# Kernel tuning notes

Hardware: AMD Instinct MI355X
Metric: run time of the kernel (lower is better)

## Reference

```python
import jax, jax.numpy as jnp
import numpy as np

B, N, D = 4, 2048, 512
H = 8            # num_heads (even)
HE = H // 2      # effective heads = 4
DH = D // H      # head_dim = 64
LAMBDA_INIT = 0.8
EPS = 1e-5


def setup_inputs() -> dict:
    key = jax.random.key(0)
    ks = jax.random.split(key, 10)
    return {
        "q": jax.random.normal(ks[0], (B, N, D), jnp.float32),
        "k": jax.random.normal(ks[1], (B, N, D), jnp.float32),
        "v": jax.random.normal(ks[2], (B, N, D), jnp.float32),
        "lambda_q1": 0.1 * jax.random.normal(ks[3], (DH,), jnp.float32),
        "lambda_k1": 0.1 * jax.random.normal(ks[4], (DH,), jnp.float32),
        "lambda_q2": 0.1 * jax.random.normal(ks[5], (DH,), jnp.float32),
        "lambda_k2": 0.1 * jax.random.normal(ks[6], (DH,), jnp.float32),
        "norm_w": jnp.ones((2 * DH,), jnp.float32),
        "out_w": 0.02 * jax.random.normal(ks[7], (D, D), jnp.float32),  # torch Linear weight [out,in]
        "out_b": jnp.zeros((D,), jnp.float32),
    }


def reference(q, k, v, lambda_q1, lambda_k1, lambda_q2, lambda_k2, norm_w, out_w, out_b):
    b, nq, d = q.shape
    nk = k.shape[1]
    # split heads: q,k -> [B, 2*HE, N, DH]; v -> [B, HE, Nk, 2*DH]
    qh = q.reshape(b, nq, 2 * HE, DH).transpose(0, 2, 1, 3) * (DH ** -0.5)
    kh = k.reshape(b, nk, 2 * HE, DH).transpose(0, 2, 1, 3)
    vh = v.reshape(b, nk, HE, 2 * DH).transpose(0, 2, 1, 3)
    scores = jnp.einsum('bhqd,bhkd->bhqk', qh, kh)          # [B, 2HE, Nq, Nk]
    probs = jax.nn.softmax(scores, axis=-1)
    probs = probs.reshape(b, HE, 2, nq, nk)
    lam = (jnp.exp(jnp.sum(lambda_q1 * lambda_k1))
           - jnp.exp(jnp.sum(lambda_q2 * lambda_k2)) + LAMBDA_INIT)
    diff = probs[:, :, 0] - lam * probs[:, :, 1]            # [B, HE, Nq, Nk]
    out = jnp.einsum('bhqk,bhkd->bhqd', diff, vh)           # [B, HE, Nq, 2*DH]
    # per-head RMSNorm over last dim (2*DH), elementwise affine
    out = out * jax.lax.rsqrt(jnp.mean(out * out, axis=-1, keepdims=True) + EPS)
    out = out * norm_w * (1.0 - LAMBDA_INIT)
    out = out.transpose(0, 2, 1, 3).reshape(b, nq, d)
    return out @ out_w.T + out_b
```

## Files before the change

kernel.cpp:

```cpp
#include <hip/hip_runtime.h>
#include <math.h>

#define BB 4
#define NN 2048
#define DD 512
#define LAMBDA_INIT 0.8f
#define EPSV 1e-5f

typedef __attribute__((ext_vector_type(8))) short bf16x8;
typedef __attribute__((ext_vector_type(4))) float f32x4;
typedef __attribute__((ext_vector_type(16))) float f32x16;
typedef unsigned short u16;
typedef __attribute__((ext_vector_type(4))) u16 u16x4;
typedef __attribute__((ext_vector_type(8))) u16 u16x8;
typedef __attribute__((ext_vector_type(4))) unsigned u32x4;

__device__ __forceinline__ u16 f2bf(float f) {
  unsigned u = __builtin_bit_cast(unsigned, f);
  u = (u + 0x7FFFu + ((u >> 16) & 1u)) >> 16;
  return (u16)u;
}

__device__ __forceinline__ void gload16(const void* g, void* l) {
  __builtin_amdgcn_global_load_lds((const __attribute__((address_space(1))) unsigned*)g,
                                   (__attribute__((address_space(3))) unsigned*)l, 16, 0, 0);
}

__device__ __forceinline__ f32x16 fz16() {
  f32x16 z;
  #pragma unroll
  for (int i = 0; i < 16; ++i) z[i] = 0.f;
  return z;
}

__device__ __forceinline__ void plswap(unsigned &a, unsigned &b) {
  asm("v_permlane32_swap_b32 %0, %1" : "+v"(a), "+v"(b));
}
__device__ __forceinline__ float xhalf_add(float x) {
  unsigned a = __builtin_bit_cast(unsigned, x), b;
  asm("v_mov_b32 %0, %1" : "=v"(b) : "v"(a));
  asm("v_permlane32_swap_b32 %0, %1" : "+v"(a), "+v"(b));
  return __builtin_bit_cast(float, a) + __builtin_bit_cast(float, b);
}

__global__ __launch_bounds__(256) void prep_kernel(
    const float* __restrict__ q, const float* __restrict__ k, const float* __restrict__ w,
    u16* __restrict__ Qb, u16* __restrict__ Kb, u16* __restrict__ Wb)
{
  const int t = threadIdx.x;
  const int bid = blockIdx.x;
  if (bid >= BB * NN) {
    const size_t idx = (size_t)(bid - BB * NN) * 256 + t;
    float4 f = *(const float4*)&w[idx * 4];
    u16x4 o = { f2bf(f.x), f2bf(f.y), f2bf(f.z), f2bf(f.w) };
    *(u16x4*)&Wb[idx * 4] = o;
    return;
  }
  const size_t row = bid;
  const int n = bid & (NN - 1);
  const int b = bid >> 11;
  if (t < 128) {
    const float s = 0.125f * 1.4426950408889634f;
    float4 f = *(const float4*)&q[row * DD + t * 4];
    u16x4 o = { f2bf(f.x * s), f2bf(f.y * s), f2bf(f.z * s), f2bf(f.w * s) };
    *(u16x4*)&Qb[row * DD + t * 4] = o;
  } else {
    const int f0 = (t - 128) * 4;
    float4 f = *(const float4*)&k[row * DD + f0];
    const int he = f0 >> 7, fi = f0 & 127;
    const int gi = fi >> 3, lo = fi & 7;
    const int gi2 = (gi & 8) | ((gi & 7) ^ (n & 7));
    u16x4 o = { f2bf(f.x), f2bf(f.y), f2bf(f.z), f2bf(f.w) };
    *(u16x4*)&Kb[((size_t)(b * 4 + he) * NN + n) * 128 + gi2 * 8 + lo] = o;
  }
}

__global__ __launch_bounds__(256) void v_prep_kernel(const float* __restrict__ v, u16* __restrict__ Vbt) {
  __shared__ u16 Ls[64][72];
  const int t = threadIdx.x;
  const int n0 = blockIdx.x * 64;
  const int d0 = blockIdx.y * 64;
  const int z  = blockIdx.z;
  #pragma unroll
  for (int p = 0; p < 4; ++p) {
    int n = p * 16 + (t >> 4), f4 = t & 15;
    float4 rv = *(const float4*)&v[((size_t)((z >> 2) * NN + n0 + n)) * DD + (z & 3) * 128 + d0 + f4 * 4];
    Ls[n][f4*4+0] = f2bf(rv.x); Ls[n][f4*4+1] = f2bf(rv.y);
    Ls[n][f4*4+2] = f2bf(rv.z); Ls[n][f4*4+3] = f2bf(rv.w);
  }
  __syncthreads();
  #pragma unroll
  for (int rep = 0; rep < 2; ++rep) {
    const int sid   = rep * 256 + t;
    const int tt    = sid >> 8;
    const int rem   = sid & 255;
    const int i_rel = rem >> 6;
    const int ls    = rem & 63;
    const int i_    = (d0 >> 4) + i_rel;
    const int j     = i_ * 8 + (ls >> 3);
    const int s0    = (ls & 7) ^ (j & 7);
    const int dl    = 2 * (i_rel * 8 + (ls >> 3)) + (s0 >> 2);
    const int nl0   = tt * 32 + (s0 & 3) * 8;
    u16x8 o;
    #pragma unroll
    for (int jj = 0; jj < 8; ++jj) o[jj] = Ls[nl0 + jj][dl];
    const int tile = blockIdx.x * 2 + tt;
    *(u16x8*)&Vbt[((size_t)z * 64 + tile) * 4096 + i_ * 512 + ls * 8] = o;
  }
}

#define ISSUE_K4(dst, kv0, hf) do { \
  _Pragma("unroll") for (int i_ = 0; i_ < 4; ++i_) { int ii_ = (hf)*4 + i_; \
    gload16(kgb + (((size_t)(kv0) + ii_ * 4 + (l >> 4)) << 7) + ((l & 15) << 3), (dst) + ii_ * 512); } \
  __builtin_amdgcn_sched_barrier(0); } while (0)

#define ISSUE_V4(dst, kv0, hf) do { \
  _Pragma("unroll") for (int i_ = 0; i_ < 4; ++i_) { int ii_ = (hf)*4 + i_; \
    gload16(vgb + ((size_t)((kv0) >> 5)) * 4096 + ii_ * 512 + l * 8, (dst) + ii_ * 512); } \
  __builtin_amdgcn_sched_barrier(0); } while (0)

#define WAIT_VM0 do { asm volatile("s_waitcnt vmcnt(0)" ::: "memory"); \
  __builtin_amdgcn_sched_barrier(0); } while (0)

__global__ __launch_bounds__(512, 2) void attn7_kernel(
    const u16* __restrict__ Qb, const u16* __restrict__ Kb, const u16* __restrict__ Vbt,
    const float* __restrict__ lq1, const float* __restrict__ lk1,
    const float* __restrict__ lq2, const float* __restrict__ lk2,
    const float* __restrict__ norm_w, u16* __restrict__ Xb)
{
  __shared__ __align__(16) u16 smem[32768];
  __shared__ float stats[2][2][2][32];

  u16* KB = smem;
  u16* VB = smem + 16384;

  const int tid = threadIdx.x;
  const int w   = tid >> 6;
  const int l   = tid & 63;
  const int hi  = l >> 5;
  const int q   = l & 31;
  const int h   = w & 1;
  const int kvh = (w >> 1) & 1;
  const int qh  = w >> 2;

  const int bid0 = blockIdx.x;
  const int bid = (bid0 & 7) * 64 + (bid0 >> 3);
  const int qt = bid & 31;
  const int he = (bid >> 5) & 3;
  const int b  = bid >> 7;
  const int q0 = qt * 64;
  const int bhe = b * 4 + he;
  const int qrow = q0 + qh * 32 + q;

  float lp1 = lq1[l] * lk1[l], lp2 = lq2[l] * lk2[l];
  #pragma unroll
  for (int off = 32; off; off >>= 1) { lp1 += __shfl_xor(lp1, off); lp2 += __shfl_xor(lp2, off); }
  const float lam = __expf(lp1) - __expf(lp2) + LAMBDA_INIT;
  asm volatile("" :: "v"(lam));

  bf16x8 qf[4];
  {
    const u16* qp = Qb + ((size_t)(b * NN) + qrow) * DD + he * 128 + h * 64 + hi * 8;
    #pragma unroll
    for (int dk = 0; dk < 4; ++dk)
      qf[dk] = *(const bf16x8*)(qp + dk * 16);
  }
  WAIT_VM0;
  #pragma unroll
  for (int dk = 0; dk < 4; ++dk)
    asm volatile("" :: "v"(qf[dk]));

  const u16* kgb = Kb + (size_t)bhe * NN * 128;
  const u16* vgb = Vbt + (size_t)bhe * 64 * 4096;
  const int kvb = kvh * 1024;

  if (h == 0) ISSUE_K4(&KB[kvh * 8192], kvb, qh);
  else        ISSUE_V4(&VB[kvh * 8192], kvb, qh);

  f32x16 O[4];
  #pragma unroll
  for (int dt = 0; dt < 4; ++dt) O[dt] = fz16();
  float sl = 0.f;

  const int jq  = (q >> 1) & 7;
  const int dq1 = (q & 1) << 2;

  #pragma unroll 2
  for (int tt = 0; tt < 32; ++tt) {
    WAIT_VM0;
    __builtin_amdgcn_s_barrier();
    __builtin_amdgcn_sched_barrier(0);

    {
      const int kvn = kvb + ((tt + 1) & 31) * 32;
      const int db = (tt + 1) & 1;
      if (h == 0) ISSUE_K4(&KB[(kvh * 2 + db) * 4096], kvn, qh);
      else        ISSUE_V4(&VB[(kvh * 2 + db) * 4096], kvn, qh);
    }

    const u16* Kcur = &KB[(kvh * 2 + (tt & 1)) * 4096];
    const u16* Vcur = &VB[(kvh * 2 + (tt & 1)) * 4096];

    f32x16 S;
    __builtin_amdgcn_s_setprio(1);
    {
      f32x16 acc = fz16();
      #pragma unroll
      for (int dk = 0; dk < 4; ++dk) {
        const int gd = h * 8 + dk * 2 + hi;
        const int g2 = (gd & 8) | ((gd & 7) ^ (q & 7));
        bf16x8 kf = *(const bf16x8*)&Kcur[q * 128 + g2 * 8];
        acc = __builtin_amdgcn_mfma_f32_32x32x16_bf16(kf, qf[dk], acc, 0, 0, 0);
      }
      S = acc;
    }
    __builtin_amdgcn_s_setprio(0);

    #pragma unroll
    for (int r = 0; r < 16; ++r)
      S[r] = __builtin_amdgcn_exp2f(S[r]);
    {
      float y0 = (S[0]  + S[1])  + (S[2]  + S[3]);
      float y1 = (S[4]  + S[5])  + (S[6]  + S[7]);
      float y2 = (S[8]  + S[9])  + (S[10] + S[11]);
      float y3 = (S[12] + S[13]) + (S[14] + S[15]);
      sl += (y0 + y1) + (y2 + y3);
    }
    bf16x8 pb[2];
    {
      unsigned PK[8];
      #pragma unroll
      for (int p2 = 0; p2 < 8; ++p2)
        asm("v_cvt_pk_bf16_f32 %0, %1, %2" : "=v"(PK[p2]) : "v"(S[2*p2]), "v"(S[2*p2+1]));
      #pragma unroll
      for (int kb = 0; kb < 2; ++kb) {
        unsigned w0 = PK[4*kb + 0], w2v = PK[4*kb + 2];
        unsigned w1 = PK[4*kb + 1], w3v = PK[4*kb + 3];
        plswap(w0, w2v);
        plswap(w1, w3v);
        union { u32x4 u; bf16x8 v; } cv;
        cv.u = (u32x4){ w0, w1, w2v, w3v };
        pb[kb] = cv.v;
      }
    }

    __builtin_amdgcn_s_setprio(1);
    #pragma unroll
    for (int kk = 0; kk < 2; ++kk)
      #pragma unroll
      for (int dt = 0; dt < 4; ++dt) {
        const int j = dt * 16 + (q >> 1);
        const int s8 = (dq1 + kk * 2 + hi) ^ jq;
        bf16x8 vf = *(const bf16x8*)&Vcur[j * 64 + s8 * 8];
        O[dt] = __builtin_amdgcn_mfma_f32_32x32x16_bf16(vf, pb[kk], O[dt], 0, 0, 0);
      }
    __builtin_amdgcn_s_setprio(0);
  }

  WAIT_VM0;
  __syncthreads();

  sl = xhalf_add(sl);
  if (hi == 0) stats[qh][h][kvh][q] = sl;
  __syncthreads();
  const float L = stats[qh][h][0][q] + stats[qh][h][1][q];

  float* xch = (float*)smem;
  if (kvh == 1) {
    #pragma unroll
    for (int dt = 0; dt < 4; ++dt)
      #pragma unroll
      for (int r = 0; r < 16; ++r)
        xch[(qh * 2 + h) * 4096 + (dt * 16 + r) * 64 + l] = O[dt][r];
  }
  __syncthreads();
  if (kvh == 0) {
    #pragma unroll
    for (int dt = 0; dt < 4; ++dt)
      #pragma unroll
      for (int r = 0; r < 16; ++r)
        O[dt][r] += xch[(qh * 2 + h) * 4096 + (dt * 16 + r) * 64 + l];
  }
  __syncthreads();
  if (kvh == 0 && h == 1) {
    const float s2 = lam / L;
    #pragma unroll
    for (int dt = 0; dt < 4; ++dt)
      #pragma unroll
      for (int r = 0; r < 16; ++r)
        xch[qh * 4096 + (dt * 16 + r) * 64 + l] = O[dt][r] * s2;
  }
  __syncthreads();
  if (kvh == 0 && h == 0) {
    const float i1 = 1.f / L;
    float ss = 0.f;
    #pragma unroll
    for (int dt = 0; dt < 4; ++dt)
      #pragma unroll
      for (int r = 0; r < 16; ++r) {
        float o = O[dt][r] * i1 - xch[qh * 4096 + (dt * 16 + r) * 64 + l];
        O[dt][r] = o;
        ss += o * o;
      }
    ss = xhalf_add(ss);
    const float rstd = rsqrtf(ss * (1.f / 128.f) + EPSV);
    const size_t xo = ((size_t)(b * NN) + qrow) * DD + he * 128;
    #pragma unroll
    for (int dt = 0; dt < 4; ++dt)
      #pragma unroll
      for (int rq = 0; rq < 4; ++rq) {
        const int d0 = dt * 32 + rq * 8 + hi * 4;
        const float4 nw = *(const float4*)&norm_w[d0];
        u16x4 ov;
        ov[0] = f2bf(O[dt][rq*4 + 0] * rstd * nw.x * 0.2f);
        ov[1] = f2bf(O[dt][rq*4 + 1] * rstd * nw.y * 0.2f);
        ov[2] = f2bf(O[dt][rq*4 + 2] * rstd * nw.z * 0.2f);
        ov[3] = f2bf(O[dt][rq*4 + 3] * rstd * nw.w * 0.2f);
        *(u16x4*)&Xb[xo + d0] = ov;
      }
  }
}

#define PLOAD(k0) do { \
    _Pragma("unroll") for (int p_ = 0; p_ < 2; ++p_) { \
      int idx_ = p_*256 + t; int r_ = idx_ >> 3, gi_ = idx_ & 7; \
      ra[p_] = *(const u16x8*)&Xb[(size_t)(row0 + r_) * DD + (k0) + gi_*8]; \
      rb[p_] = *(const u16x8*)&Wb[(size_t)(col0 + r_) * DD + (k0) + gi_*8]; } \
  } while (0)
#define PWRITE(bi) do { \
    _Pragma("unroll") for (int p_ = 0; p_ < 2; ++p_) { \
      int idx_ = p_*256 + t; int r_ = idx_ >> 3, gi_ = idx_ & 7; \
      *(u16x8*)&As[bi][r_*64 + ((gi_ ^ (r_ & 7)) << 3)] = ra[p_]; \
      *(u16x8*)&Bs[bi][r_*64 + ((gi_ ^ (r_ & 7)) << 3)] = rb[p_]; } \
  } while (0)

__global__ __launch_bounds__(256, 2) void proj_mfma_kernel(
    const u16* __restrict__ Xb, const u16* __restrict__ Wb,
    const float* __restrict__ bias, float* __restrict__ out)
{
  __shared__ __align__(16) u16 As[2][64*64];
  __shared__ __align__(16) u16 Bs[2][64*64];
  const int t = threadIdx.x;
  const int w = t >> 6, l = t & 63, g = l >> 4, c = l & 15;
  const int wm = w >> 1, wn = w & 1;
  const int row0 = blockIdx.x * 64, col0 = blockIdx.y * 64;

  u16x8 ra[2], rb[2];
  f32x4 acc[2][2];
  #pragma unroll
  for (int i = 0; i < 2; ++i)
    #pragma unroll
    for (int j = 0; j < 2; ++j) acc[i][j] = (f32x4){0,0,0,0};
  float bj[2];
  #pragma unroll
  for (int j = 0; j < 2; ++j) bj[j] = bias[col0 + wn*32 + j*16 + c];

  PLOAD(0);
  PWRITE(0);
  __syncthreads();
  for (int s = 0; s < 8; ++s) {
    const int bi = s & 1;
    if (s < 7) PLOAD((s + 1) * 64);
    #pragma unroll
    for (int kc = 0; kc < 2; ++kc) {
      bf16x8 af[2], bfv[2];
      #pragma unroll
      for (int i = 0; i < 2; ++i) {
        int rowa = wm*32 + i*16 + c;
        af[i]  = *(const bf16x8*)&As[bi][rowa*64 + (((kc*4 + g) ^ (c & 7)) << 3)];
        int rowb = wn*32 + i*16 + c;
        bfv[i] = *(const bf16x8*)&Bs[bi][rowb*64 + (((kc*4 + g) ^ (c & 7)) << 3)];
      }
      #pragma unroll
      for (int i = 0; i < 2; ++i)
        #pragma unroll
        for (int j = 0; j < 2; ++j)
          acc[i][j] = __builtin_amdgcn_mfma_f32_16x16x32_bf16(af[i], bfv[j], acc[i][j], 0, 0, 0);
    }
    if (s < 7) PWRITE((s + 1) & 1);
    __syncthreads();
  }
  #pragma unroll
  for (int i = 0; i < 2; ++i)
    #pragma unroll
    for (int j = 0; j < 2; ++j)
      #pragma unroll
      for (int rr = 0; rr < 4; ++rr)
        out[(size_t)(row0 + wm*32 + i*16 + g*4 + rr) * DD + col0 + wn*32 + j*16 + c] = acc[i][j][rr] + bj[j];
}

extern "C" void kernel_launch(void* const* d_in, const int* in_sizes, int n_in,
                              void* d_out, int out_size, void* d_ws, size_t ws_size,
                              hipStream_t stream) {
    const float* q      = (const float*)d_in[0];
    const float* k      = (const float*)d_in[1];
    const float* v      = (const float*)d_in[2];
    const float* lq1    = (const float*)d_in[3];
    const float* lk1    = (const float*)d_in[4];
    const float* lq2    = (const float*)d_in[5];
    const float* lk2    = (const float*)d_in[6];
    const float* norm_w = (const float*)d_in[7];
    const float* out_w  = (const float*)d_in[8];
    const float* out_b  = (const float*)d_in[9];
    float* out = (float*)d_out;

    u16* Qb  = (u16*)d_ws;
    u16* Kb  = (u16*)((char*)d_ws + (8u  << 20));
    u16* Vbt = (u16*)((char*)d_ws + (16u << 20));
    u16* Wb  = (u16*)((char*)d_ws + (24u << 20));
    u16* Xb  = (u16*)((char*)d_ws + (25u << 20));

    prep_kernel<<<BB * NN + 256, 256, 0, stream>>>(q, k, out_w, Qb, Kb, Wb);
    v_prep_kernel<<<dim3(32, 2, 16), 256, 0, stream>>>(v, Vbt);
    attn7_kernel<<<512, 512, 0, stream>>>(Qb, Kb, Vbt, lq1, lk1, lq2, lk2, norm_w, Xb);
    proj_mfma_kernel<<<dim3(128, 8), 256, 0, stream>>>(Xb, Wb, out_b, out);
}
```

Baseline: 106.7 us.

## Process two query groups per wave to reuse K/V fragments

The attention kernel drops from 8 to 4 waves per block, and each wave now handles both 32-row query groups. Each K and V fragment read from LDS feeds two MFMAs, which halves LDS read traffic per MFMA. The price is doubled accumulator registers, fewer waves available to hide latency, and more complex cross-wave exchange indexing in the epilogue. The loop unroll pragma is removed, likely to limit register pressure.

```diff
diff --git a/kernel.cpp b/kernel.cpp
--- a/kernel.cpp
+++ b/kernel.cpp
@@ -109,20 +109,20 @@
   }
 }
 
-#define ISSUE_K4(dst, kv0, hf) do { \
-  _Pragma("unroll") for (int i_ = 0; i_ < 4; ++i_) { int ii_ = (hf)*4 + i_; \
-    gload16(kgb + (((size_t)(kv0) + ii_ * 4 + (l >> 4)) << 7) + ((l & 15) << 3), (dst) + ii_ * 512); } \
+#define ISSUE_K8(dst, kv0) do { \
+  _Pragma("unroll") for (int i_ = 0; i_ < 8; ++i_) \
+    gload16(kgb + (((size_t)(kv0) + i_ * 4 + (l >> 4)) << 7) + ((l & 15) << 3), (dst) + i_ * 512); \
   __builtin_amdgcn_sched_barrier(0); } while (0)
 
-#define ISSUE_V4(dst, kv0, hf) do { \
-  _Pragma("unroll") for (int i_ = 0; i_ < 4; ++i_) { int ii_ = (hf)*4 + i_; \
-    gload16(vgb + ((size_t)((kv0) >> 5)) * 4096 + ii_ * 512 + l * 8, (dst) + ii_ * 512); } \
+#define ISSUE_V8(dst, kv0) do { \
+  _Pragma("unroll") for (int i_ = 0; i_ < 8; ++i_) \
+    gload16(vgb + ((size_t)((kv0) >> 5)) * 4096 + i_ * 512 + l * 8, (dst) + i_ * 512); \
   __builtin_amdgcn_sched_barrier(0); } while (0)
 
 #define WAIT_VM0 do { asm volatile("s_waitcnt vmcnt(0)" ::: "memory"); \
   __builtin_amdgcn_sched_barrier(0); } while (0)
 
-__global__ __launch_bounds__(512, 2) void attn7_kernel(
+__global__ __launch_bounds__(256, 2) void attn8_kernel(
     const u16* __restrict__ Qb, const u16* __restrict__ Kb, const u16* __restrict__ Vbt,
     const float* __restrict__ lq1, const float* __restrict__ lk1,
     const float* __restrict__ lq2, const float* __restrict__ lk2,
@@ -139,9 +139,8 @@
   const int l   = tid & 63;
   const int hi  = l >> 5;
   const int q   = l & 31;
-  const int h   = w & 1;
-  const int kvh = (w >> 1) & 1;
-  const int qh  = w >> 2;
+  const int h   = w >> 1;
+  const int kvh = w & 1;
 
   const int bid0 = blockIdx.x;
   const int bid = (bid0 & 7) * 64 + (bid0 >> 3);
@@ -150,7 +149,6 @@
   const int b  = bid >> 7;
   const int q0 = qt * 64;
   const int bhe = b * 4 + he;
-  const int qrow = q0 + qh * 32 + q;
 
   float lp1 = lq1[l] * lk1[l], lp2 = lq2[l] * lk2[l];
   #pragma unroll
@@ -158,34 +156,38 @@
   const float lam = __expf(lp1) - __expf(lp2) + LAMBDA_INIT;
   asm volatile("" :: "v"(lam));
 
-  bf16x8 qf[4];
-  {
-    const u16* qp = Qb + ((size_t)(b * NN) + qrow) * DD + he * 128 + h * 64 + hi * 8;
+  bf16x8 qf[2][4];
+  #pragma unroll
+  for (int g = 0; g < 2; ++g) {
+    const u16* qp = Qb + ((size_t)(b * NN) + q0 + g * 32 + q) * DD + he * 128 + h * 64 + hi * 8;
     #pragma unroll
     for (int dk = 0; dk < 4; ++dk)
-      qf[dk] = *(const bf16x8*)(qp + dk * 16);
+      qf[g][dk] = *(const bf16x8*)(qp + dk * 16);
   }
   WAIT_VM0;
   #pragma unroll
-  for (int dk = 0; dk < 4; ++dk)
-    asm volatile("" :: "v"(qf[dk]));
+  for (int g = 0; g < 2; ++g)
+    #pragma unroll
+    for (int dk = 0; dk < 4; ++dk)
+      asm volatile("" :: "v"(qf[g][dk]));
 
   const u16* kgb = Kb + (size_t)bhe * NN * 128;
   const u16* vgb = Vbt + (size_t)bhe * 64 * 4096;
   const int kvb = kvh * 1024;
 
-  if (h == 0) ISSUE_K4(&KB[kvh * 8192], kvb, qh);
-  else        ISSUE_V4(&VB[kvh * 8192], kvb, qh);
-
-  f32x16 O[4];
-  #pragma unroll
-  for (int dt = 0; dt < 4; ++dt) O[dt] = fz16();
-  float sl = 0.f;
+  if (h == 0) ISSUE_K8(&KB[kvh * 8192], kvb);
+  else        ISSUE_V8(&VB[kvh * 8192], kvb);
+
+  f32x16 O[2][4];
+  #pragma unroll
+  for (int g = 0; g < 2; ++g)
+    #pragma unroll
+    for (int dt = 0; dt < 4; ++dt) O[g][dt] = fz16();
+  float sl[2] = {0.f, 0.f};
 
   const int jq  = (q >> 1) & 7;
   const int dq1 = (q & 1) << 2;
 
-  #pragma unroll 2
   for (int tt = 0; tt < 32; ++tt) {
     WAIT_VM0;
     __builtin_amdgcn_s_barrier();
@@ -194,44 +196,46 @@
     {
       const int kvn = kvb + ((tt + 1) & 31) * 32;
       const int db = (tt + 1) & 1;
-      if (h == 0) ISSUE_K4(&KB[(kvh * 2 + db) * 4096], kvn, qh);
-      else        ISSUE_V4(&VB[(kvh * 2 + db) * 4096], kvn, qh);
+      if (h == 0) ISSUE_K8(&KB[(kvh * 2 + db) * 4096], kvn);
+      else        ISSUE_V8(&VB[(kvh * 2 + db) * 4096], kvn);
     }
 
     const u16* Kcur = &KB[(kvh * 2 + (tt & 1)) * 4096];
     const u16* Vcur = &VB[(kvh * 2 + (tt & 1)) * 4096];
 
-    f32x16 S;
+    f32x16 Sg[2];
     __builtin_amdgcn_s_setprio(1);
     {
-      f32x16 acc = fz16();
+      f32x16 a0 = fz16(), a1 = fz16();
       #pragma unroll
       for (int dk = 0; dk < 4; ++dk) {
         const int gd = h * 8 + dk * 2 + hi;
         const int g2 = (gd & 8) | ((gd & 7) ^ (q & 7));
         bf16x8 kf = *(const bf16x8*)&Kcur[q * 128 + g2 * 8];
-        acc = __builtin_amdgcn_mfma_f32_32x32x16_bf16(kf, qf[dk], acc, 0, 0, 0);
+        a0 = __builtin_amdgcn_mfma_f32_32x32x16_bf16(kf, qf[0][dk], a0, 0, 0, 0);
+        a1 = __builtin_amdgcn_mfma_f32_32x32x16_bf16(kf, qf[1][dk], a1, 0, 0, 0);
       }
-      S = acc;
+      Sg[0] = a0; Sg[1] = a1;
     }
     __builtin_amdgcn_s_setprio(0);
 
-    #pragma unroll
-    for (int r = 0; r < 16; ++r)
-      S[r] = __builtin_amdgcn_exp2f(S[r]);
-    {
-      float y0 = (S[0]  + S[1])  + (S[2]  + S[3]);
-      float y1 = (S[4]  + S[5])  + (S[6]  + S[7]);
-      float y2 = (S[8]  + S[9])  + (S[10] + S[11]);
-      float y3 = (S[12] + S[13]) + (S[14] + S[15]);
-      sl += (y0 + y1) + (y2 + y3);
-    }
-    bf16x8 pb[2];
-    {
+    bf16x8 pb[2][2];
+    #pragma unroll
+    for (int g = 0; g < 2; ++g) {
+      #pragma unroll
+      for (int r = 0; r < 16; ++r)
+        Sg[g][r] = __builtin_amdgcn_exp2f(Sg[g][r]);
+      {
+        float y0 = (Sg[g][0]  + Sg[g][1])  + (Sg[g][2]  + Sg[g][3]);
+        float y1 = (Sg[g][4]  + Sg[g][5])  + (Sg[g][6]  + Sg[g][7]);
+        float y2 = (Sg[g][8]  + Sg[g][9])  + (Sg[g][10] + Sg[g][11]);
+        float y3 = (Sg[g][12] + Sg[g][13]) + (Sg[g][14] + Sg[g][15]);
+        sl[g] += (y0 + y1) + (y2 + y3);
+      }
       unsigned PK[8];
       #pragma unroll
       for (int p2 = 0; p2 < 8; ++p2)
-        asm("v_cvt_pk_bf16_f32 %0, %1, %2" : "=v"(PK[p2]) : "v"(S[2*p2]), "v"(S[2*p2+1]));
+        asm("v_cvt_pk_bf16_f32 %0, %1, %2" : "=v"(PK[p2]) : "v"(Sg[g][2*p2]), "v"(Sg[g][2*p2+1]));
       #pragma unroll
       for (int kb = 0; kb < 2; ++kb) {
         unsigned w0 = PK[4*kb + 0], w2v = PK[4*kb + 2];
@@ -240,7 +244,7 @@
         plswap(w1, w3v);
         union { u32x4 u; bf16x8 v; } cv;
         cv.u = (u32x4){ w0, w1, w2v, w3v };
-        pb[kb] = cv.v;
+        pb[g][kb] = cv.v;
       }
     }
 
@@ -252,7 +256,8 @@
         const int j = dt * 16 + (q >> 1);
         const int s8 = (dq1 + kk * 2 + hi) ^ jq;
         bf16x8 vf = *(const bf16x8*)&Vcur[j * 64 + s8 * 8];
-        O[dt] = __builtin_amdgcn_mfma_f32_32x32x16_bf16(vf, pb[kk], O[dt], 0, 0, 0);
+        O[0][dt] = __builtin_amdgcn_mfma_f32_32x32x16_bf16(vf, pb[0][kk], O[0][dt], 0, 0, 0);
+        O[1][dt] = __builtin_amdgcn_mfma_f32_32x32x16_bf16(vf, pb[1][kk], O[1][dt], 0, 0, 0);
       }
     __builtin_amdgcn_s_setprio(0);
   }
@@ -260,64 +265,84 @@
   WAIT_VM0;
   __syncthreads();
 
-  sl = xhalf_add(sl);
-  if (hi == 0) stats[qh][h][kvh][q] = sl;
-  __syncthreads();
-  const float L = stats[qh][h][0][q] + stats[qh][h][1][q];
+  #pragma unroll
+  for (int g = 0; g < 2; ++g) sl[g] = xhalf_add(sl[g]);
+  if (hi == 0) { stats[h][kvh][0][q] = sl[0]; stats[h][kvh][1][q] = sl[1]; }
+  __syncthreads();
+  float L[2];
+  #pragma unroll
+  for (int g = 0; g < 2; ++g) L[g] = stats[h][0][g][q] + stats[h][1][g][q];
 
   float* xch = (float*)smem;
   if (kvh == 1) {
     #pragma unroll
-    for (int dt = 0; dt < 4; ++dt)
-      #pragma unroll
-      for (int r = 0; r < 16; ++r)
-        xch[(qh * 2 + h) * 4096 + (dt * 16 + r) * 64 + l] = O[dt][r];
+    for (int g = 0; g < 2; ++g)
+      #pragma unroll
+      for (int dt = 0; dt < 4; ++dt)
+        #pragma unroll
+        for (int r = 0; r < 16; ++r) {
+          const int crow = (r & 3) + 8 * (r >> 2) + 4 * hi;
+          xch[h * 8192 + (dt * 32 + crow) * 64 + g * 32 + q] = O[g][dt][r];
+        }
   }
   __syncthreads();
   if (kvh == 0) {
     #pragma unroll
-    for (int dt = 0; dt < 4; ++dt)
-      #pragma unroll
-      for (int r = 0; r < 16; ++r)
-        O[dt][r] += xch[(qh * 2 + h) * 4096 + (dt * 16 + r) * 64 + l];
+    for (int g = 0; g < 2; ++g)
+      #pragma unroll
+      for (int dt = 0; dt < 4; ++dt)
+        #pragma unroll
+        for (int r = 0; r < 16; ++r) {
+          const int crow = (r & 3) + 8 * (r >> 2) + 4 * hi;
+          O[g][dt][r] += xch[h * 8192 + (dt * 32 + crow) * 64 + g * 32 + q];
+        }
   }
   __syncthreads();
   if (kvh == 0 && h == 1) {
-    const float s2 = lam / L;
-    #pragma unroll
-    for (int dt = 0; dt < 4; ++dt)
-      #pragma unroll
-      for (int r = 0; r < 16; ++r)
-        xch[qh * 4096 + (dt * 16 + r) * 64 + l] = O[dt][r] * s2;
+    #pragma unroll
+    for (int g = 0; g < 2; ++g) {
+      const float s2 = lam / L[g];
+      #pragma unroll
+      for (int dt = 0; dt < 4; ++dt)
+        #pragma unroll
+        for (int r = 0; r < 16; ++r) {
+          const int crow = (r & 3) + 8 * (r >> 2) + 4 * hi;
+          xch[(dt * 32 + crow) * 64 + g * 32 + q] = O[g][dt][r] * s2;
+        }
+    }
   }
   __syncthreads();
   if (kvh == 0 && h == 0) {
-    const float i1 = 1.f / L;
-    float ss = 0.f;
-    #pragma unroll
-    for (int dt = 0; dt < 4; ++dt)
-      #pragma unroll
-      for (int r = 0; r < 16; ++r) {
-        float o = O[dt][r] * i1 - xch[qh * 4096 + (dt * 16 + r) * 64 + l];
-        O[dt][r] = o;
-        ss += o * o;
-      }
-    ss = xhalf_add(ss);
-    const float rstd = rsqrtf(ss * (1.f / 128.f) + EPSV);
-    const size_t xo = ((size_t)(b * NN) + qrow) * DD + he * 128;
-    #pragma unroll
-    for (int dt = 0; dt < 4; ++dt)
-      #pragma unroll
-      for (int rq = 0; rq < 4; ++rq) {
-        const int d0 = dt * 32 + rq * 8 + hi * 4;
-        const float4 nw = *(const float4*)&norm_w[d0];
-        u16x4 ov;
-        ov[0] = f2bf(O[dt][rq*4 + 0] * rstd * nw.x * 0.2f);
-        ov[1] = f2bf(O[dt][rq*4 + 1] * rstd * nw.y * 0.2f);
-        ov[2] = f2bf(O[dt][rq*4 + 2] * rstd * nw.z * 0.2f);
-        ov[3] = f2bf(O[dt][rq*4 + 3] * rstd * nw.w * 0.2f);
-        *(u16x4*)&Xb[xo + d0] = ov;
-      }
+    #pragma unroll
+    for (int g = 0; g < 2; ++g) {
+      const float i1 = 1.f / L[g];
+      float ss = 0.f;
+      #pragma unroll
+      for (int dt = 0; dt < 4; ++dt)
+        #pragma unroll
+        for (int r = 0; r < 16; ++r) {
+          const int crow = (r & 3) + 8 * (r >> 2) + 4 * hi;
+          float o = O[g][dt][r] * i1 - xch[(dt * 32 + crow) * 64 + g * 32 + q];
+          O[g][dt][r] = o;
+          ss += o * o;
+        }
+      ss = xhalf_add(ss);
+      const float rstd = rsqrtf(ss * (1.f / 128.f) + EPSV);
+      const size_t xo = ((size_t)(b * NN) + q0 + g * 32 + q) * DD + he * 128;
+      #pragma unroll
+      for (int dt = 0; dt < 4; ++dt)
+        #pragma unroll
+        for (int rq = 0; rq < 4; ++rq) {
+          const int d0 = dt * 32 + rq * 8 + hi * 4;
+          const float4 nw = *(const float4*)&norm_w[d0];
+          u16x4 ov;
+          ov[0] = f2bf(O[g][dt][rq*4 + 0] * rstd * nw.x * 0.2f);
+          ov[1] = f2bf(O[g][dt][rq*4 + 1] * rstd * nw.y * 0.2f);
+          ov[2] = f2bf(O[g][dt][rq*4 + 2] * rstd * nw.z * 0.2f);
+          ov[3] = f2bf(O[g][dt][rq*4 + 3] * rstd * nw.w * 0.2f);
+          *(u16x4*)&Xb[xo + d0] = ov;
+        }
+    }
   }
 }
 
@@ -412,6 +437,6 @@
 
     prep_kernel<<<BB * NN + 256, 256, 0, stream>>>(q, k, out_w, Qb, Kb, Wb);
     v_prep_kernel<<<dim3(32, 2, 16), 256, 0, stream>>>(v, Vbt);
-    attn7_kernel<<<512, 512, 0, stream>>>(Qb, Kb, Vbt, lq1, lk1, lq2, lk2, norm_w, Xb);
+    attn8_kernel<<<512, 256, 0, stream>>>(Qb, Kb, Vbt, lq1, lk1, lq2, lk2, norm_w, Xb);
     proj_mfma_kernel<<<dim3(128, 8), 256, 0, stream>>>(Xb, Wb, out_b, out);
 }
```

After: 96.53 us. -9.5%, faster.
